# Kernel tuning notes

Measured on AMD Instinct MI355X. Metric: run time of the kernel, lower is better.

The kernel has to match this reference:

```python
import jax, jax.numpy as jnp
import numpy as np

N, E, F_IN, EMB = 100000, 1600000, 64, 64


def _glorot(key, shape):
    fan_in, fan_out = shape[1], shape[0]
    lim = (6.0 / (fan_in + fan_out)) ** 0.5
    return jax.random.uniform(key, shape, jnp.float32, -lim, lim)


def setup_inputs() -> dict:
    key = jax.random.key(0)
    ks = jax.random.split(key, 24)
    inp = {
        "x": jax.random.normal(ks[0], (N, F_IN), jnp.float32),
        "edge_index": jax.random.randint(ks[1], (2, E), 0, N, jnp.int64),
        "edge_attr": jax.random.uniform(ks[2], (E, 1), jnp.float32),
        "h1": jnp.zeros((N, EMB), jnp.float32),
        "h2": jnp.zeros((N, EMB), jnp.float32),
        # SAGEConv 1: lin_l (aggregated neighbors, with bias), lin_r (root, no bias)
        "sage1_lW": _glorot(ks[3], (EMB, F_IN)), "sage1_lb": jnp.zeros((EMB,), jnp.float32),
        "sage1_rW": _glorot(ks[4], (EMB, F_IN)),
        "sage2_lW": _glorot(ks[5], (EMB, EMB)), "sage2_lb": jnp.zeros((EMB,), jnp.float32),
        "sage2_rW": _glorot(ks[6], (EMB, EMB)),
        # GraphNorm params (weight, bias, mean_scale)
        "gn1_w": jnp.ones((EMB,), jnp.float32), "gn1_b": jnp.zeros((EMB,), jnp.float32), "gn1_ms": jnp.ones((EMB,), jnp.float32),
        "gn2_w": jnp.ones((EMB,), jnp.float32), "gn2_b": jnp.zeros((EMB,), jnp.float32), "gn2_ms": jnp.ones((EMB,), jnp.float32),
        # GRUCell 1: input 2*EMB -> EMB ; GRUCell 2: EMB -> EMB (torch layout: [3*H, in])
        "gru1_wih": _glorot(ks[7], (3 * EMB, 2 * EMB)), "gru1_whh": _glorot(ks[8], (3 * EMB, EMB)),
        "gru1_bih": jnp.zeros((3 * EMB,), jnp.float32), "gru1_bhh": jnp.zeros((3 * EMB,), jnp.float32),
        "gru2_wih": _glorot(ks[9], (3 * EMB, EMB)), "gru2_whh": _glorot(ks[10], (3 * EMB, EMB)),
        "gru2_bih": jnp.zeros((3 * EMB,), jnp.float32), "gru2_bhh": jnp.zeros((3 * EMB,), jnp.float32),
        "day_idx": 0,
    }
    return inp


def _sage(x, src, dst, ew, lW, lb, rW, n_nodes):
    # message = edge_weight * x_j, aggr = mean over incoming edges at dst
    msg = x[src] * ew                                   # [E, F]
    agg = jax.ops.segment_sum(msg, dst, num_segments=n_nodes)
    cnt = jax.ops.segment_sum(jnp.ones((src.shape[0], 1), x.dtype), dst, num_segments=n_nodes)
    agg = agg / jnp.maximum(cnt, 1.0)
    return agg @ lW.T + lb + x @ rW.T


def _graph_norm(x, w, b, ms, eps=1e-5):
    mean = jnp.mean(x, axis=0, keepdims=True)           # single graph -> global node mean
    out = x - ms * mean
    var = jnp.mean(out * out, axis=0, keepdims=True)
    return w * out * jax.lax.rsqrt(var + eps) + b


def _gru_cell(x, h, wih, whh, bih, bhh):
    gi = x @ wih.T + bih                                # [N, 3H]
    gh = h @ whh.T + bhh
    ir, iz, in_ = jnp.split(gi, 3, axis=1)
    hr, hz, hn = jnp.split(gh, 3, axis=1)
    r = jax.nn.sigmoid(ir + hr)
    z = jax.nn.sigmoid(iz + hz)
    n = jnp.tanh(in_ + r * hn)
    return (1.0 - z) * n + z * h


def reference(x, edge_index, edge_attr, h1, h2,
              sage1_lW, sage1_lb, sage1_rW, sage2_lW, sage2_lb, sage2_rW,
              gn1_w, gn1_b, gn1_ms, gn2_w, gn2_b, gn2_ms,
              gru1_wih, gru1_whh, gru1_bih, gru1_bhh,
              gru2_wih, gru2_whh, gru2_bih, gru2_bhh, day_idx):
    src, dst = edge_index[0], edge_index[1]
    n_nodes = x.shape[0]
    x1 = jax.nn.relu(_graph_norm(_sage(x, src, dst, edge_attr, sage1_lW, sage1_lb, sage1_rW, n_nodes), gn1_w, gn1_b, gn1_ms))
    x2 = jax.nn.relu(_graph_norm(_sage(x1, src, dst, edge_attr, sage2_lW, sage2_lb, sage2_rW, n_nodes), gn2_w, gn2_b, gn2_ms))
    xc = jnp.concatenate([x1, x2], axis=1)              # [N, 2*EMB]
    h1n = _gru_cell(xc, h1, gru1_wih, gru1_whh, gru1_bih, gru1_bhh)
    h2n = _gru_cell(h1n, h2, gru2_wih, gru2_whh, gru2_bih, gru2_bhh)
    return (xc, h1n, h2n)
```

## Files before the change

### kernel.cpp

```cpp
#include <hip/hip_runtime.h>
#include <hip/hip_bf16.h>


typedef short  s16x8 __attribute__((ext_vector_type(8)));
typedef float  f32x4 __attribute__((ext_vector_type(4)));

#define MFMA16(a,b,c) __builtin_amdgcn_mfma_f32_16x16x32_bf16((a),(b),(c),0,0,0)
#define SCAN_TILE 4096

__device__ __forceinline__ unsigned short f2b(float f){
  __hip_bfloat16 h = __float2bfloat16(f);
  return *reinterpret_cast<unsigned short*>(&h);
}
__device__ __forceinline__ float b2f(unsigned short u){
  __hip_bfloat16 h = *reinterpret_cast<__hip_bfloat16*>(&u);
  return __bfloat162float(h);
}
__device__ __forceinline__ s16x8 ld8(const unsigned short* p){
  return *reinterpret_cast<const s16x8*>(p);
}
__device__ __forceinline__ s16x8 cvt8(const float* p){
  float4 a = *reinterpret_cast<const float4*>(p);
  float4 b = *reinterpret_cast<const float4*>(p+4);
  s16x8 r;
  r[0]=(short)f2b(a.x); r[1]=(short)f2b(a.y); r[2]=(short)f2b(a.z); r[3]=(short)f2b(a.w);
  r[4]=(short)f2b(b.x); r[5]=(short)f2b(b.y); r[6]=(short)f2b(b.z); r[7]=(short)f2b(b.w);
  return r;
}
__device__ __forceinline__ float sigf(float x){ return 1.f/(1.f+__expf(-x)); }
__device__ __forceinline__ float tanhf_(float x){ return 1.f - 2.f/(1.f+__expf(2.f*x)); }

__global__ void k_count(const int* __restrict__ ei, int E, int* __restrict__ deg){
  int e = blockIdx.x*256 + threadIdx.x;
  if(e<E) atomicAdd(&deg[ei[E+e]], 1);
}

__global__ __launch_bounds__(256) void k_scan1(const int* __restrict__ deg, int N,
                                               int* __restrict__ bsum){
  __shared__ int sh[256];
  int b = blockIdx.x, t = threadIdx.x;
  int i0 = b*SCAN_TILE + t*16;
  int s = 0;
  #pragma unroll
  for(int i=0;i<16;i++){ int idx=i0+i; if(idx<N) s+=deg[idx]; }
  sh[t]=s; __syncthreads();
  for(int off=128; off>0; off>>=1){ if(t<off) sh[t]+=sh[t+off]; __syncthreads(); }
  if(t==0) bsum[b]=sh[0];
}

__global__ void k_scan2(int* __restrict__ bsum, int nb){
  __shared__ int sh[1024];
  int t = threadIdx.x;
  int v = (t<nb)? bsum[t] : 0;
  sh[t]=v; __syncthreads();
  for(int off=1; off<1024; off<<=1){
    int u = (t>=off)? sh[t-off] : 0;
    __syncthreads();
    sh[t]+=u;
    __syncthreads();
  }
  if(t<nb) bsum[t] = sh[t]-v;
}

__global__ __launch_bounds__(256) void k_scan3(const int* __restrict__ deg, int N, int E,
                                               const int* __restrict__ bsum,
                                               int* __restrict__ rowptr, int* __restrict__ cursor){
  __shared__ int sh[256];
  int b = blockIdx.x, t = threadIdx.x;
  int i0 = b*SCAN_TILE + t*16;
  int local[16];
  int s = 0;
  #pragma unroll
  for(int i=0;i<16;i++){
    int idx=i0+i;
    int d = (idx<N)? deg[idx] : 0;
    local[i]=d; s+=d;
  }
  sh[t]=s; __syncthreads();
  for(int off=1; off<256; off<<=1){
    int u = (t>=off)? sh[t-off] : 0;
    __syncthreads();
    sh[t]+=u;
    __syncthreads();
  }
  int run = bsum[b] + sh[t]-s;
  #pragma unroll
  for(int i=0;i<16;i++){
    int idx=i0+i;
    if(idx<N){ rowptr[idx]=run; cursor[idx]=run; run+=local[i]; }
  }
  if(b==0 && t==0) rowptr[N]=E;
}

__global__ void k_fill(const int* __restrict__ ei, const float* __restrict__ ea, int E,
                       int* __restrict__ cursor, int* __restrict__ srcs,
                       unsigned short* __restrict__ ewb){
  int e = blockIdx.x*256 + threadIdx.x;
  if(e<E){
    int d = ei[E+e];
    int p = atomicAdd(&cursor[d], 1);
    srcs[p] = ei[e];
    ewb[p]  = f2b(ea[e]);
  }
}

__global__ void k_prep_w(const float* __restrict__ a0, const float* __restrict__ a1,
                         const float* __restrict__ a2, const float* __restrict__ a3,
                         const float* __restrict__ a4, const float* __restrict__ a5,
                         const float* __restrict__ a6, const float* __restrict__ a7,
                         unsigned short* __restrict__ out){
  int i = blockIdx.x*256 + threadIdx.x;
  const float* src; int off;
  if      (i< 4096){ src=a0; off=0;     }
  else if (i< 8192){ src=a1; off=4096;  }
  else if (i<12288){ src=a2; off=8192;  }
  else if (i<16384){ src=a3; off=12288; }
  else if (i<40960){ src=a4; off=16384; }
  else if (i<53248){ src=a5; off=40960; }
  else if (i<65536){ src=a6; off=53248; }
  else if (i<77824){ src=a7; off=65536; }
  else return;
  out[i] = f2b(src[i-off]);
}

__global__ void k_aggregate(const float* __restrict__ xin, int ldx,
                            const int* __restrict__ rowptr,
                            const int* __restrict__ srcs, const unsigned short* __restrict__ ewb,
                            int N, unsigned short* __restrict__ aggb){
  int node = blockIdx.x*4 + (threadIdx.x>>6);
  int lane = threadIdx.x & 63;
  if(node>=N) return;
  int b = rowptr[node], e = rowptr[node+1];
  float acc = 0.f;
  int i = b;
  for(; i+4<=e; i+=4){
    int s0=srcs[i], s1=srcs[i+1], s2=srcs[i+2], s3=srcs[i+3];
    float w0=b2f(ewb[i]),  w1=b2f(ewb[i+1]), w2=b2f(ewb[i+2]), w3=b2f(ewb[i+3]);
    float v0=xin[(size_t)s0*ldx+lane], v1=xin[(size_t)s1*ldx+lane];
    float v2=xin[(size_t)s2*ldx+lane], v3=xin[(size_t)s3*ldx+lane];
    acc = fmaf(v0,w0,acc); acc = fmaf(v1,w1,acc);
    acc = fmaf(v2,w2,acc); acc = fmaf(v3,w3,acc);
  }
  for(; i<e; i++)
    acc = fmaf(xin[(size_t)srcs[i]*ldx+lane], b2f(ewb[i]), acc);
  acc *= 1.f/(float)max(e-b, 1);
  aggb[(size_t)node*64 + lane] = f2b(acc);
}

__global__ __launch_bounds__(256) void k_sage_mfma(
    const unsigned short* __restrict__ aggb,
    const float* __restrict__ xin, int ldx,
    const unsigned short* __restrict__ lWb,
    const unsigned short* __restrict__ rWb,
    const float* __restrict__ lb,
    int N, float* __restrict__ sbuf,
    float* __restrict__ gsum, float* __restrict__ gsq){
  __shared__ float red[2][4][64];
  int tid = threadIdx.x;
  int wid = tid>>6, lane = tid&63;
  int l15 = lane&15, lk = lane>>4;
  int m0 = blockIdx.x*64 + wid*16;
  int arow = min(m0 + l15, N-1);
  f32x4 acc[4];
  #pragma unroll
  for(int c=0;c<4;c++) acc[c] = (f32x4){0.f,0.f,0.f,0.f};

  #pragma unroll
  for(int kt=0; kt<2; kt++){
    s16x8 a = ld8(&aggb[(size_t)arow*64 + kt*32 + lk*8]);
    #pragma unroll
    for(int c=0;c<4;c++){
      s16x8 b = ld8(&lWb[(size_t)(c*16+l15)*64 + kt*32 + lk*8]);
      acc[c] = MFMA16(a,b,acc[c]);
    }
  }
  #pragma unroll
  for(int kt=0; kt<2; kt++){
    s16x8 a = cvt8(&xin[(size_t)arow*ldx + kt*32 + lk*8]);
    #pragma unroll
    for(int c=0;c<4;c++){
      s16x8 b = ld8(&rWb[(size_t)(c*16+l15)*64 + kt*32 + lk*8]);
      acc[c] = MFMA16(a,b,acc[c]);
    }
  }
  float ssum[4], ssq[4];
  #pragma unroll
  for(int c=0;c<4;c++){
    int col = c*16 + l15;
    float bias = lb[col];
    float s_=0.f, q_=0.f;
    #pragma unroll
    for(int r=0;r<4;r++){
      int row = m0 + lk*4 + r;
      if(row<N){
        float v = acc[c][r] + bias;
        sbuf[(size_t)row*64 + col] = v;
        s_ += v; q_ += v*v;
      }
    }
    ssum[c]=s_; ssq[c]=q_;
  }
  #pragma unroll
  for(int c=0;c<4;c++){
    ssum[c] += __shfl_xor(ssum[c],16); ssum[c] += __shfl_xor(ssum[c],32);
    ssq[c]  += __shfl_xor(ssq[c],16);  ssq[c]  += __shfl_xor(ssq[c],32);
  }
  if(lk==0){
    #pragma unroll
    for(int c=0;c<4;c++){
      red[0][wid][c*16+l15] = ssum[c];
      red[1][wid][c*16+l15] = ssq[c];
    }
  }
  __syncthreads();
  if(tid<64){
    float a = red[0][0][tid]+red[0][1][tid]+red[0][2][tid]+red[0][3][tid];
    float b = red[1][0][tid]+red[1][1][tid]+red[1][2][tid]+red[1][3][tid];
    atomicAdd(&gsum[tid], a);
    atomicAdd(&gsq[tid],  b);
  }
}

__global__ void k_norm_fin(const float* __restrict__ gsum, const float* __restrict__ gsq,
                           const float* __restrict__ w, const float* __restrict__ b,
                           const float* __restrict__ ms,
                           float Ninv, float* __restrict__ alpha, float* __restrict__ beta){
  int j = threadIdx.x;
  float m   = gsum[j]*Ninv;
  float ex2 = gsq[j]*Ninv;
  float msv = ms[j];
  float var = ex2 - m*m*msv*(2.f-msv);
  float rinv = rsqrtf(var + 1e-5f);
  float a = w[j]*rinv;
  alpha[j] = a;
  beta[j]  = b[j] - a*msv*m;
}

__global__ void k_apply(const float* __restrict__ sbuf, const float* __restrict__ ab,
                        int N, float* __restrict__ outbase){
  int t = blockIdx.x*256 + threadIdx.x;
  int total = N*16;
  if(t>=total) return;
  int node = t>>4, q = t&15;
  float4 s  = *reinterpret_cast<const float4*>(&sbuf[(size_t)node*64 + q*4]);
  float4 al = *reinterpret_cast<const float4*>(&ab[q*4]);
  float4 be = *reinterpret_cast<const float4*>(&ab[64 + q*4]);
  float4 o;
  o.x = fmaxf(fmaf(s.x,al.x,be.x), 0.f);
  o.y = fmaxf(fmaf(s.y,al.y,be.y), 0.f);
  o.z = fmaxf(fmaf(s.z,al.z,be.z), 0.f);
  o.w = fmaxf(fmaf(s.w,al.w,be.w), 0.f);
  *reinterpret_cast<float4*>(&outbase[(size_t)node*128 + q*4]) = o;
}

__global__ __launch_bounds__(256) void k_gru_mfma(
    const float* __restrict__ xin, int ldx, int K1,
    const float* __restrict__ hin,
    const unsigned short* __restrict__ wihb,
    const unsigned short* __restrict__ whhb,
    const float* __restrict__ bih, const float* __restrict__ bhh,
    int N, float* __restrict__ hout){
  int tid = threadIdx.x;
  int wid = tid>>6, lane = tid&63;
  int l15 = lane&15, lk = lane>>4;
  int m0 = blockIdx.x*16;
  int c0 = wid*16;
  int arow = min(m0 + l15, N-1);
  f32x4 ai[3], ah[3];
  #pragma unroll
  for(int g=0;g<3;g++){ ai[g]=(f32x4){0.f,0.f,0.f,0.f}; ah[g]=(f32x4){0.f,0.f,0.f,0.f}; }

  for(int kt=0; kt<K1/32; kt++){
    s16x8 a = cvt8(&xin[(size_t)arow*ldx + kt*32 + lk*8]);
    #pragma unroll
    for(int g=0; g<3; g++){
      s16x8 b = ld8(&wihb[(size_t)(g*64 + c0 + l15)*K1 + kt*32 + lk*8]);
      ai[g] = MFMA16(a,b,ai[g]);
    }
  }
  #pragma unroll
  for(int kt=0; kt<2; kt++){
    s16x8 a = cvt8(&hin[(size_t)arow*64 + kt*32 + lk*8]);
    #pragma unroll
    for(int g=0; g<3; g++){
      s16x8 b = ld8(&whhb[(size_t)(g*64 + c0 + l15)*64 + kt*32 + lk*8]);
      ah[g] = MFMA16(a,b,ah[g]);
    }
  }
  int j = c0 + l15;
  float bi_r=bih[j], bi_z=bih[64+j], bi_n=bih[128+j];
  float bh_r=bhh[j], bh_z=bhh[64+j], bh_n=bhh[128+j];
  #pragma unroll
  for(int r=0;r<4;r++){
    int row = m0 + lk*4 + r;
    if(row<N){
      float hp = hin[(size_t)row*64 + j];
      float rg = sigf(ai[0][r]+bi_r + ah[0][r]+bh_r);
      float z  = sigf(ai[1][r]+bi_z + ah[1][r]+bh_z);
      float n  = tanhf_(fmaf(rg, ah[2][r]+bh_n, ai[2][r]+bi_n));
      hout[(size_t)row*64 + j] = fmaf(z, hp-n, n);
    }
  }
}

extern "C" void kernel_launch(void* const* d_in, const int* in_sizes, int n_in,
                              void* d_out, int out_size, void* d_ws, size_t ws_size,
                              hipStream_t stream) {
  const float* x    = (const float*)d_in[0];
  const int*   ei   = (const int*)d_in[1];
  const float* ea   = (const float*)d_in[2];
  const float* h1   = (const float*)d_in[3];
  const float* h2   = (const float*)d_in[4];
  const float* s1lW = (const float*)d_in[5];
  const float* s1lb = (const float*)d_in[6];
  const float* s1rW = (const float*)d_in[7];
  const float* s2lW = (const float*)d_in[8];
  const float* s2lb = (const float*)d_in[9];
  const float* s2rW = (const float*)d_in[10];
  const float* gn1w = (const float*)d_in[11];
  const float* gn1b = (const float*)d_in[12];
  const float* gn1ms= (const float*)d_in[13];
  const float* gn2w = (const float*)d_in[14];
  const float* gn2b = (const float*)d_in[15];
  const float* gn2ms= (const float*)d_in[16];
  const float* g1wih= (const float*)d_in[17];
  const float* g1whh= (const float*)d_in[18];
  const float* g1bih= (const float*)d_in[19];
  const float* g1bhh= (const float*)d_in[20];
  const float* g2wih= (const float*)d_in[21];
  const float* g2whh= (const float*)d_in[22];
  const float* g2bih= (const float*)d_in[23];
  const float* g2bhh= (const float*)d_in[24];

  int N = in_sizes[0]/64;
  int E = in_sizes[2];
  if(N<=0) return;

  char* base = (char*)d_ws;
  size_t off = 0;
  float* gsum1 = (float*)(base);
  float* gsq1  = gsum1 + 64;
  float* gsum2 = gsum1 + 128;
  float* gsq2  = gsum1 + 192;
  float* ab1   = gsum1 + 256;
  float* ab2   = gsum1 + 384;
  off = 512*4;
  int nb_scan = (N + SCAN_TILE-1)/SCAN_TILE;
  int* bsum   = (int*)(base+off); off += 1024*4;
  int* deg    = (int*)(base+off); off += (size_t)N*4;
  int* rowptr = (int*)(base+off); off += ((size_t)N+1)*4;
  int* cursor = (int*)(base+off); off += (size_t)N*4;
  int* srcs   = (int*)(base+off); off += (size_t)E*4;
  unsigned short* ewb = (unsigned short*)(base+off); off += (size_t)E*2;
  off = (off + 63) & ~(size_t)63;
  unsigned short* wbf = (unsigned short*)(base+off);
  unsigned short* s1lWb = wbf;
  unsigned short* s1rWb = wbf + 4096;
  unsigned short* s2lWb = wbf + 8192;
  unsigned short* s2rWb = wbf + 12288;
  unsigned short* g1wihb= wbf + 16384;
  unsigned short* g1whhb= wbf + 40960;
  unsigned short* g2wihb= wbf + 53248;
  unsigned short* g2whhb= wbf + 65536;

  float* xc  = (float*)d_out;
  float* h1n = xc + (size_t)N*128;
  float* h2n = h1n + (size_t)N*64;
  float* sbuf = h1n;
  unsigned short* aggb = (unsigned short*)h2n;

  hipMemsetAsync(gsum1, 0, 512*4, stream);
  hipMemsetAsync(deg, 0, (size_t)N*4, stream);

  int eb  = (E+255)/256;
  k_count<<<eb,256,0,stream>>>(ei, E, deg);
  k_scan1<<<nb_scan,256,0,stream>>>(deg, N, bsum);
  k_scan2<<<1,1024,0,stream>>>(bsum, nb_scan);
  k_scan3<<<nb_scan,256,0,stream>>>(deg, N, E, bsum, rowptr, cursor);
  k_fill <<<eb,256,0,stream>>>(ei, ea, E, cursor, srcs, ewb);
  k_prep_w<<<(77824+255)/256,256,0,stream>>>(s1lW,s1rW,s2lW,s2rW,g1wih,g1whh,g2wih,g2whh, wbf);

  int nb4 = (N+3)/4;
  int gb  = (N+63)/64;
  int apb = (N*16+255)/256;
  int grb = (N+15)/16;

  k_aggregate<<<nb4,256,0,stream>>>(x, 64, rowptr, srcs, ewb, N, aggb);
  k_sage_mfma<<<gb,256,0,stream>>>(aggb, x, 64, s1lWb, s1rWb, s1lb, N, sbuf, gsum1, gsq1);
  k_norm_fin<<<1,64,0,stream>>>(gsum1, gsq1, gn1w, gn1b, gn1ms, 1.f/(float)N, ab1, ab1+64);
  k_apply<<<apb,256,0,stream>>>(sbuf, ab1, N, xc);

  k_aggregate<<<nb4,256,0,stream>>>(xc, 128, rowptr, srcs, ewb, N, aggb);
  k_sage_mfma<<<gb,256,0,stream>>>(aggb, xc, 128, s2lWb, s2rWb, s2lb, N, sbuf, gsum2, gsq2);
  k_norm_fin<<<1,64,0,stream>>>(gsum2, gsq2, gn2w, gn2b, gn2ms, 1.f/(float)N, ab2, ab2+64);
  k_apply<<<apb,256,0,stream>>>(sbuf, ab2, N, xc + 64);

  k_gru_mfma<<<grb,256,0,stream>>>(xc, 128, 128, h1, g1wihb, g1whhb, g1bih, g1bhh, N, h1n);
  k_gru_mfma<<<grb,256,0,stream>>>(h1n, 64, 64,  h2, g2wihb, g2whhb, g2bih, g2bhh, N, h2n);
}
```

Measured before the change: 784.6 us.

## Gather bf16 node features and pack edge src/weight into 64-bit records

```diff
diff --git a/kernel.cpp b/kernel.cpp
--- a/kernel.cpp
+++ b/kernel.cpp
@@ -93,14 +93,13 @@
 }
 
 __global__ void k_fill(const int* __restrict__ ei, const float* __restrict__ ea, int E,
-                       int* __restrict__ cursor, int* __restrict__ srcs,
-                       unsigned short* __restrict__ ewb){
+                       int* __restrict__ cursor, unsigned long long* __restrict__ erec){
   int e = blockIdx.x*256 + threadIdx.x;
   if(e<E){
     int d = ei[E+e];
     int p = atomicAdd(&cursor[d], 1);
-    srcs[p] = ei[e];
-    ewb[p]  = f2b(ea[e]);
+    unsigned long long w = (unsigned long long)f2b(ea[e]);
+    erec[p] = (unsigned long long)(unsigned int)ei[e] | (w<<32);
   }
 }
 
@@ -123,9 +122,17 @@
   out[i] = f2b(src[i-off]);
 }
 
-__global__ void k_aggregate(const float* __restrict__ xin, int ldx,
+__global__ void k_xb16(const float* __restrict__ x, int total8,
+                       unsigned short* __restrict__ xb){
+  int i = blockIdx.x*256 + threadIdx.x;
+  if(i>=total8) return;
+  s16x8 v = cvt8(&x[(size_t)i*8]);
+  *reinterpret_cast<s16x8*>(&xb[(size_t)i*8]) = v;
+}
+
+__global__ void k_aggregate(const unsigned short* __restrict__ xb,
                             const int* __restrict__ rowptr,
-                            const int* __restrict__ srcs, const unsigned short* __restrict__ ewb,
+                            const unsigned long long* __restrict__ erec,
                             int N, unsigned short* __restrict__ aggb){
   int node = blockIdx.x*4 + (threadIdx.x>>6);
   int lane = threadIdx.x & 63;
@@ -134,15 +141,21 @@
   float acc = 0.f;
   int i = b;
   for(; i+4<=e; i+=4){
-    int s0=srcs[i], s1=srcs[i+1], s2=srcs[i+2], s3=srcs[i+3];
-    float w0=b2f(ewb[i]),  w1=b2f(ewb[i+1]), w2=b2f(ewb[i+2]), w3=b2f(ewb[i+3]);
-    float v0=xin[(size_t)s0*ldx+lane], v1=xin[(size_t)s1*ldx+lane];
-    float v2=xin[(size_t)s2*ldx+lane], v3=xin[(size_t)s3*ldx+lane];
+    unsigned long long r0=erec[i], r1=erec[i+1], r2=erec[i+2], r3=erec[i+3];
+    int s0=(int)(r0&0xffffffffu), s1=(int)(r1&0xffffffffu);
+    int s2=(int)(r2&0xffffffffu), s3=(int)(r3&0xffffffffu);
+    float w0=b2f((unsigned short)(r0>>32)), w1=b2f((unsigned short)(r1>>32));
+    float w2=b2f((unsigned short)(r2>>32)), w3=b2f((unsigned short)(r3>>32));
+    float v0=b2f(xb[(size_t)s0*64+lane]), v1=b2f(xb[(size_t)s1*64+lane]);
+    float v2=b2f(xb[(size_t)s2*64+lane]), v3=b2f(xb[(size_t)s3*64+lane]);
     acc = fmaf(v0,w0,acc); acc = fmaf(v1,w1,acc);
     acc = fmaf(v2,w2,acc); acc = fmaf(v3,w3,acc);
   }
-  for(; i<e; i++)
-    acc = fmaf(xin[(size_t)srcs[i]*ldx+lane], b2f(ewb[i]), acc);
+  for(; i<e; i++){
+    unsigned long long r = erec[i];
+    int s=(int)(r&0xffffffffu);
+    acc = fmaf(b2f(xb[(size_t)s*64+lane]), b2f((unsigned short)(r>>32)), acc);
+  }
   acc *= 1.f/(float)max(e-b, 1);
   aggb[(size_t)node*64 + lane] = f2b(acc);
 }
@@ -237,7 +250,8 @@
 }
 
 __global__ void k_apply(const float* __restrict__ sbuf, const float* __restrict__ ab,
-                        int N, float* __restrict__ outbase){
+                        int N, float* __restrict__ outbase,
+                        unsigned short* __restrict__ yb16){
   int t = blockIdx.x*256 + threadIdx.x;
   int total = N*16;
   if(t>=total) return;
@@ -251,6 +265,11 @@
   o.z = fmaxf(fmaf(s.z,al.z,be.z), 0.f);
   o.w = fmaxf(fmaf(s.w,al.w,be.w), 0.f);
   *reinterpret_cast<float4*>(&outbase[(size_t)node*128 + q*4]) = o;
+  if(yb16){
+    ushort4 u;
+    u.x = f2b(o.x); u.y = f2b(o.y); u.z = f2b(o.z); u.w = f2b(o.w);
+    *reinterpret_cast<ushort4*>(&yb16[(size_t)node*64 + q*4]) = u;
+  }
 }
 
 __global__ __launch_bounds__(256) void k_gru_mfma(
@@ -350,9 +369,8 @@
   int* deg    = (int*)(base+off); off += (size_t)N*4;
   int* rowptr = (int*)(base+off); off += ((size_t)N+1)*4;
   int* cursor = (int*)(base+off); off += (size_t)N*4;
-  int* srcs   = (int*)(base+off); off += (size_t)E*4;
-  unsigned short* ewb = (unsigned short*)(base+off); off += (size_t)E*2;
-  off = (off + 63) & ~(size_t)63;
+  off = (off + 7) & ~(size_t)7;
+  unsigned long long* erec = (unsigned long long*)(base+off); off += (size_t)E*8;
   unsigned short* wbf = (unsigned short*)(base+off);
   unsigned short* s1lWb = wbf;
   unsigned short* s1rWb = wbf + 4096;
@@ -368,6 +386,7 @@
   float* h2n = h1n + (size_t)N*64;
   float* sbuf = h1n;
   unsigned short* aggb = (unsigned short*)h2n;
+  unsigned short* xb16 = aggb + (size_t)N*64;
 
   hipMemsetAsync(gsum1, 0, 512*4, stream);
   hipMemsetAsync(deg, 0, (size_t)N*4, stream);
@@ -377,23 +396,25 @@
   k_scan1<<<nb_scan,256,0,stream>>>(deg, N, bsum);
   k_scan2<<<1,1024,0,stream>>>(bsum, nb_scan);
   k_scan3<<<nb_scan,256,0,stream>>>(deg, N, E, bsum, rowptr, cursor);
-  k_fill <<<eb,256,0,stream>>>(ei, ea, E, cursor, srcs, ewb);
+  k_fill <<<eb,256,0,stream>>>(ei, ea, E, cursor, erec);
   k_prep_w<<<(77824+255)/256,256,0,stream>>>(s1lW,s1rW,s2lW,s2rW,g1wih,g1whh,g2wih,g2whh, wbf);
+  int t8 = N*64/8;
+  k_xb16<<<(t8+255)/256,256,0,stream>>>(x, t8, xb16);
 
   int nb4 = (N+3)/4;
   int gb  = (N+63)/64;
   int apb = (N*16+255)/256;
   int grb = (N+15)/16;
 
-  k_aggregate<<<nb4,256,0,stream>>>(x, 64, rowptr, srcs, ewb, N, aggb);
+  k_aggregate<<<nb4,256,0,stream>>>(xb16, rowptr, erec, N, aggb);
   k_sage_mfma<<<gb,256,0,stream>>>(aggb, x, 64, s1lWb, s1rWb, s1lb, N, sbuf, gsum1, gsq1);
   k_norm_fin<<<1,64,0,stream>>>(gsum1, gsq1, gn1w, gn1b, gn1ms, 1.f/(float)N, ab1, ab1+64);
-  k_apply<<<apb,256,0,stream>>>(sbuf, ab1, N, xc);
-
-  k_aggregate<<<nb4,256,0,stream>>>(xc, 128, rowptr, srcs, ewb, N, aggb);
+  k_apply<<<apb,256,0,stream>>>(sbuf, ab1, N, xc, xb16);
+
+  k_aggregate<<<nb4,256,0,stream>>>(xb16, rowptr, erec, N, aggb);
   k_sage_mfma<<<gb,256,0,stream>>>(aggb, xc, 128, s2lWb, s2rWb, s2lb, N, sbuf, gsum2, gsq2);
   k_norm_fin<<<1,64,0,stream>>>(gsum2, gsq2, gn2w, gn2b, gn2ms, 1.f/(float)N, ab2, ab2+64);
-  k_apply<<<apb,256,0,stream>>>(sbuf, ab2, N, xc + 64);
+  k_apply<<<apb,256,0,stream>>>(sbuf, ab2, N, xc + 64, (unsigned short*)nullptr);
 
   k_gru_mfma<<<grb,256,0,stream>>>(xc, 128, 128, h1, g1wihb, g1whhb, g1bih, g1bhh, N, h1n);
   k_gru_mfma<<<grb,256,0,stream>>>(h1n, 64, 64,  h2, g2wihb, g2whhb, g2bih, g2bhh, N, h2n);
```

New measurement: 795.1 us. No clear change (+1.3%).
